# Kernel tuning notes

Measured on AMD Instinct MI355X. Metric: run time of the kernel, lower is better.

## Reference

```python
import jax, jax.numpy as jnp
import numpy as np

D_MODEL = 1024


def setup_inputs() -> dict:
    key = jax.random.key(0)
    kx, kq, kk, kv = jax.random.split(key, 4)
    x = jax.random.normal(kx, (4, 2048, D_MODEL), dtype=jnp.float32)
    s = 1.0 / np.sqrt(D_MODEL)
    # torch nn.Linear weight is [out, in]; y = x @ W.T
    Wq = jax.random.normal(kq, (D_MODEL, D_MODEL), dtype=jnp.float32) * s
    Wk = jax.random.normal(kk, (D_MODEL, D_MODEL), dtype=jnp.float32) * s
    Wv = jax.random.normal(kv, (D_MODEL, D_MODEL), dtype=jnp.float32) * s
    return {"x": x, "Wq": Wq, "Wk": Wk, "Wv": Wv}


def reference(x, Wq, Wk, Wv):
    # Linear projections (no bias): [b, s, d]
    Q = jnp.einsum("bsd,ed->bse", x, Wq)
    K = jnp.einsum("bsd,ed->bse", x, Wk)
    V = jnp.einsum("bsd,ed->bse", x, Wv)
    d_k = Q.shape[-1]
    scores = jnp.einsum("bqd,bkd->bqk", Q, K) / jnp.sqrt(jnp.asarray(d_k, Q.dtype))
    weights = jax.nn.softmax(scores, axis=-1)
    return jnp.einsum("bqk,bkd->bqd", weights, V)
```

## Files before the change

kernel.cpp:

```cpp
#include <hip/hip_runtime.h>
#include <hip/hip_bf16.h>

using bf16 = __hip_bfloat16;
typedef __attribute__((ext_vector_type(8))) short short8;
typedef __attribute__((ext_vector_type(16))) float f32x16;

__global__ __launch_bounds__(256) void cast_all(const float* __restrict__ x,
                                                const float* __restrict__ Wq,
                                                const float* __restrict__ Wk,
                                                const float* __restrict__ Wv,
                                                bf16* __restrict__ xb, bf16* __restrict__ Wb) {
  const int b = blockIdx.x;
  const float* src;
  bf16* dst;
  if (b < 8192) {
    src = x + (size_t)b * 1024;
    dst = xb + (size_t)b * 1024;
  } else if (b < 9216) {
    src = Wq + (size_t)(b - 8192) * 1024;
    dst = Wb + (size_t)(b - 8192) * 1024;
  } else if (b < 10240) {
    src = Wk + (size_t)(b - 9216) * 1024;
    dst = Wb + (size_t)(b - 8192) * 1024;
  } else {
    src = Wv + (size_t)(b - 10240) * 1024;
    dst = Wb + (size_t)(b - 8192) * 1024;
  }
  const int i = threadIdx.x * 4;
  const float4 f = *(const float4*)(src + i);
  bf16 h[4];
  h[0] = __float2bfloat16(f.x);
  h[1] = __float2bfloat16(f.y);
  h[2] = __float2bfloat16(f.z);
  h[3] = __float2bfloat16(f.w);
  *(uint2*)(dst + i) = *(const uint2*)h;
}

#define GPHASE(AS, BS, Q, S0, S1, VM)                                          \
  do {                                                                         \
    short8 af[4], bv[2];                                                       \
    _Pragma("unroll") for (int mt = 0; mt < 4; ++mt) {                         \
      const int row = wr * 128 + mt * 32 + rl;                                 \
      const int fz = (row + (row >> 2)) & 3;                                   \
      af[mt] = *(const short8*)((AS) + row * 32 + ((((Q)*2 + grp) ^ fz) << 3));\
    }                                                                          \
    _Pragma("unroll") for (int nt = 0; nt < 2; ++nt) {                         \
      const int row = wc * 64 + nt * 32 + rl;                                  \
      const int fz = (row + (row >> 2)) & 3;                                   \
      bv[nt] = *(const short8*)((BS) + row * 32 + ((((Q)*2 + grp) ^ fz) << 3));\
    }                                                                          \
    S0;                                                                        \
    S1;                                                                        \
    VM;                                                                        \
    __builtin_amdgcn_s_barrier();                                              \
    asm volatile("s_waitcnt lgkmcnt(0)" ::: "memory");                         \
    __builtin_amdgcn_sched_barrier(0);                                         \
    __builtin_amdgcn_s_setprio(1);                                             \
    _Pragma("unroll") for (int mt = 0; mt < 4; ++mt)                           \
      _Pragma("unroll") for (int nt = 0; nt < 2; ++nt)                         \
        acc[mt][nt] = __builtin_amdgcn_mfma_f32_32x32x16_bf16(af[mt], bv[nt],  \
                                                              acc[mt][nt], 0, 0, 0); \
    __builtin_amdgcn_s_setprio(0);                                             \
    __builtin_amdgcn_s_barrier();                                              \
  } while (0)

template <class Epi>
__device__ __forceinline__ void gemm256(const bf16* __restrict__ A, const bf16* __restrict__ B,
                                        int lda, int ldb, int K, int m0, int n0, Epi epi) {
  __shared__ char smem[131072];
  const int t = threadIdx.x;
  const int lane = t & 63;
  const int wave = t >> 6;
  const int wr = wave >> 2;
  const int wc = wave & 3;
  const int rl = lane & 31;
  const int grp = lane >> 5;

  f32x16 acc[4][2];
#pragma unroll
  for (int i = 0; i < 4; ++i)
#pragma unroll
    for (int j = 0; j < 2; ++j)
#pragma unroll
      for (int r = 0; r < 16; ++r) acc[i][j][r] = 0.f;

  const bf16* gA[2];
  const bf16* gB[2];
#pragma unroll
  for (int h = 0; h < 2; ++h) {
    const int row = h * 128 + (t >> 2);
    const int fz = (row + (row >> 2)) & 3;
    const int c = ((t & 3) ^ fz) << 3;
    gA[h] = A + (size_t)(m0 + row) * lda + c;
    gB[h] = B + (size_t)(n0 + row) * ldb + c;
  }

  const int NT = K >> 5;

  auto stageA = [&](int kt, int h) {
    char* dst = smem + (((kt & 3) * 2048 + h * 512 + wave * 64) << 4);
    __builtin_amdgcn_global_load_lds(
        (const __attribute__((address_space(1))) unsigned int*)(gA[h] + kt * 32),
        (__attribute__((address_space(3))) unsigned int*)dst, 16, 0, 0);
  };
  auto stageB = [&](int kt, int h) {
    char* dst = smem + (((kt & 3) * 2048 + 1024 + h * 512 + wave * 64) << 4);
    __builtin_amdgcn_global_load_lds(
        (const __attribute__((address_space(1))) unsigned int*)(gB[h] + kt * 32),
        (__attribute__((address_space(3))) unsigned int*)dst, 16, 0, 0);
  };

  stageA(0, 0); stageB(0, 0); stageA(0, 1); stageB(0, 1);
  stageA(1, 0); stageB(1, 0); stageA(1, 1); stageB(1, 1);
  stageA(2, 0); stageB(2, 0); stageA(2, 1); stageB(2, 1);
  asm volatile("s_waitcnt vmcnt(8)" ::: "memory");
  __builtin_amdgcn_s_barrier();

  for (int kt = 0; kt < NT; ++kt) {
    const bf16* As = (const bf16*)(smem + (kt & 3) * 32768);
    const bf16* Bs = (const bf16*)(smem + (kt & 3) * 32768 + 16384);
    const bool pre = (kt + 3 < NT);
    GPHASE(As, Bs, 0, if (pre) stageA(kt + 3, 0), if (pre) stageB(kt + 3, 0), ((void)0));
    GPHASE(As, Bs, 1, if (pre) stageA(kt + 3, 1), if (pre) stageB(kt + 3, 1),
           asm volatile("s_waitcnt vmcnt(8)" ::: "memory"));
  }
  __syncthreads();

  epi(acc, m0, n0, wr, wc, lane, (char*)smem);
}

__device__ __forceinline__ int c_row(int reg, int lane) {
  return (reg & 3) + 8 * (reg >> 2) + 4 * (lane >> 5);
}

template <class F>
__device__ __forceinline__ void for_each_c(const f32x16 (&acc)[4][2], int wr, int wc, int lane,
                                           F f) {
  const int rl = lane & 31;
#pragma unroll
  for (int mt = 0; mt < 4; ++mt)
#pragma unroll
    for (int nt = 0; nt < 2; ++nt)
#pragma unroll
      for (int reg = 0; reg < 16; ++reg)
        f(wr * 128 + mt * 32 + c_row(reg, lane), wc * 64 + nt * 32 + rl, acc[mt][nt][reg]);
}

__global__ __launch_bounds__(512, 2) void proj_kernel(const bf16* __restrict__ xb,
                                                      const bf16* __restrict__ Wb,
                                                      bf16* __restrict__ Qb,
                                                      bf16* __restrict__ Kb,
                                                      bf16* __restrict__ Vt) {
  const int id = blockIdx.x;
  const int g = id & 7, s = id >> 3;
  const int m0 = (g * 4 + (s & 3)) * 256;
  const int n0 = (s >> 2) * 256;
  gemm256(xb, Wb, 1024, 1024, 1024, m0, n0,
          [=](const f32x16 (&acc)[4][2], int m0, int n0, int wr, int wc, int lane, char* smem) {
    if (n0 < 2048) {
      bf16* dst = (n0 < 1024) ? Qb : Kb;
      const int nb = n0 & 1023;
      for_each_c(acc, wr, wc, lane, [&](int m, int n, float v) {
        dst[(size_t)(m0 + m) * 1024 + nb + n] = __float2bfloat16(v);
      });
    } else {
      const int wave = threadIdx.x >> 6;
      bf16* T = (bf16*)smem + wave * 4352;
      const int rl = lane & 31;
      const int g4 = 4 * (lane >> 5);
      const int mbase = m0 + wr * 128;
      const int bb = mbase >> 11;
      const int sbase = mbase & 2047;
      const int nvbase = n0 - 2048 + wc * 64;
#pragma unroll
      for (int p = 0; p < 2; ++p) {
#pragma unroll
        for (int mt = 0; mt < 4; ++mt)
#pragma unroll
          for (int q = 0; q < 4; ++q) {
            bf16 h4[4];
#pragma unroll
            for (int r = 0; r < 4; ++r) h4[r] = __float2bfloat16(acc[mt][p][4 * q + r]);
            *(uint2*)(T + rl * 136 + mt * 32 + 8 * q + g4) = *(const uint2*)h4;
          }
        asm volatile("s_waitcnt lgkmcnt(0)" ::: "memory");
#pragma unroll
        for (int i = 0; i < 8; ++i) {
          const int nl = i * 4 + (lane >> 4);
          const int ml = (lane & 15) * 8;
          const short8 val = *(const short8*)(T + nl * 136 + ml);
          *(short8*)(Vt + ((size_t)bb * 1024 + nvbase + p * 32 + nl) * 2048 + sbase + ml) = val;
        }
        asm volatile("s_waitcnt lgkmcnt(0)" ::: "memory");
      }
    }
  });
}

__global__ __launch_bounds__(512, 2) void qk_exp_kernel(const bf16* __restrict__ Qb,
                                                        const bf16* __restrict__ Kb,
                                                        bf16* __restrict__ E,
                                                        float* __restrict__ Lpart) {
  const int z = blockIdx.y;
  const int id2 = blockIdx.x;
  const int g = id2 & 7, s = id2 >> 3;
  const int m0 = ((g & 3) * 2 + (s & 1)) * 256;
  const int n0 = ((g >> 2) * 4 + (s >> 1)) * 256;
  const bf16* A = Qb + (size_t)z * 2048 * 1024;
  const bf16* B = Kb + (size_t)z * 2048 * 1024;
  bf16* Ez = E + (size_t)z * 2048 * 2048;
  float* Lz = Lpart + (size_t)z * 8 * 2048;
  gemm256(A, B, 1024, 1024, 1024, m0, n0,
          [=](const f32x16 (&acc)[4][2], int m0, int n0, int wr, int wc, int lane, char* smem) {
    float* Lp = (float*)smem;
    const int rl = lane & 31;
#pragma unroll
    for (int mt = 0; mt < 4; ++mt)
#pragma unroll
      for (int reg = 0; reg < 16; ++reg) {
        const int mr = wr * 128 + mt * 32 + c_row(reg, lane);
        float s2 = 0.f;
#pragma unroll
        for (int nt = 0; nt < 2; ++nt) {
          const float e = __expf(acc[mt][nt][reg] * 0.03125f);
          Ez[(size_t)(m0 + mr) * 2048 + n0 + wc * 64 + nt * 32 + rl] = __float2bfloat16(e);
          s2 += e;
        }
        s2 += __shfl_xor(s2, 1, 64);
        s2 += __shfl_xor(s2, 2, 64);
        s2 += __shfl_xor(s2, 4, 64);
        s2 += __shfl_xor(s2, 8, 64);
        s2 += __shfl_xor(s2, 16, 64);
        if (rl == 0) Lp[mr * 4 + wc] = s2;
      }
    __syncthreads();
    const int t = threadIdx.x;
    if (t < 256)
      Lz[(n0 >> 8) * 2048 + m0 + t] = Lp[t * 4 + 0] + Lp[t * 4 + 1] + Lp[t * 4 + 2] + Lp[t * 4 + 3];
  });
}

__global__ __launch_bounds__(512, 2) void pv_kernel(const bf16* __restrict__ E,
                                                    const bf16* __restrict__ Vt,
                                                    const float* __restrict__ Lpart,
                                                    float* __restrict__ out) {
  const int z = blockIdx.y;
  const int id2 = blockIdx.x;
  const int g = id2 & 7, s = id2 >> 3;
  const int m0 = ((g & 3) * 2 + (s & 1)) * 256;
  const int n0 = ((g >> 2) * 2 + (s >> 1)) * 256;
  const bf16* A = E + (size_t)z * 2048 * 2048;
  const bf16* B = Vt + (size_t)z * 1024 * 2048;
  const float* Lz = Lpart + (size_t)z * 8 * 2048;
  float* oz = out + (size_t)z * 2048 * 1024;
  gemm256(A, B, 2048, 2048, 2048, m0, n0,
          [=](const f32x16 (&acc)[4][2], int m0, int n0, int wr, int wc, int lane, char* smem) {
    float* Lsm = (float*)smem;
    const int t = threadIdx.x;
    if (t < 256) {
      float s2 = 0.f;
#pragma unroll
      for (int i = 0; i < 8; ++i) s2 += Lz[(size_t)i * 2048 + m0 + t];
      Lsm[t] = 1.f / s2;
    }
    __syncthreads();
    const int rl = lane & 31;
#pragma unroll
    for (int mt = 0; mt < 4; ++mt)
#pragma unroll
      for (int reg = 0; reg < 16; ++reg) {
        const int ml = wr * 128 + mt * 32 + c_row(reg, lane);
        const float il = Lsm[ml];
#pragma unroll
        for (int nt = 0; nt < 2; ++nt)
          oz[(size_t)(m0 + ml) * 1024 + n0 + wc * 64 + nt * 32 + rl] = acc[mt][nt][reg] * il;
      }
  });
}

extern "C" void kernel_launch(void* const* d_in, const int* in_sizes, int n_in,
                              void* d_out, int out_size, void* d_ws, size_t ws_size,
                              hipStream_t stream) {
  const float* x = (const float*)d_in[0];
  const float* Wq = (const float*)d_in[1];
  const float* Wk = (const float*)d_in[2];
  const float* Wv = (const float*)d_in[3];
  float* out = (float*)d_out;

  char* w = (char*)d_ws;
  bf16* xb = (bf16*)w; w += (size_t)8192 * 1024 * 2;
  bf16* Wb = (bf16*)w; w += (size_t)3072 * 1024 * 2;
  bf16* Qb = (bf16*)w; w += (size_t)8192 * 1024 * 2;
  bf16* Kb = (bf16*)w; w += (size_t)8192 * 1024 * 2;
  bf16* Vt = (bf16*)w; w += (size_t)8192 * 1024 * 2;
  bf16* E  = (bf16*)w; w += (size_t)4 * 2048 * 2048 * 2;
  float* Lpart = (float*)w; w += (size_t)4 * 8 * 2048 * 4;

  cast_all<<<11264, 256, 0, stream>>>(x, Wq, Wk, Wv, xb, Wb);

  proj_kernel<<<384, 512, 0, stream>>>(xb, Wb, Qb, Kb, Vt);

  qk_exp_kernel<<<dim3(64, 4), 512, 0, stream>>>(Qb, Kb, E, Lpart);

  pv_kernel<<<dim3(32, 4), 512, 0, stream>>>(E, Vt, Lpart, out);
}
```

Before: 261.6 us.

## Restructure GEMM mainloop into 64-wide K tiles with 4-phase double-buffered schedule

Replaces the 4-stage, 32-wide-K pipeline with a double-buffered 64-wide-K scheme. Each K tile is split into four MFMA quadrants, and the A/B half-tile loads for the next tiles are interleaved between them. Each wave's rows are remapped to two 64-row halves, so the epilogues and the V-transpose staging buffer change to match. The aim is fewer barriers and better overlap of LDS reads, global-to-LDS loads and MFMA work, at the cost of more register pressure and more complex wait-count bookkeeping.

After: 255.4 us. 2.4% less time.

```diff
diff --git a/kernel.cpp b/kernel.cpp
--- a/kernel.cpp
+++ b/kernel.cpp
@@ -36,33 +36,11 @@
   *(uint2*)(dst + i) = *(const uint2*)h;
 }
 
-#define GPHASE(AS, BS, Q, S0, S1, VM)                                          \
-  do {                                                                         \
-    short8 af[4], bv[2];                                                       \
-    _Pragma("unroll") for (int mt = 0; mt < 4; ++mt) {                         \
-      const int row = wr * 128 + mt * 32 + rl;                                 \
-      const int fz = (row + (row >> 2)) & 3;                                   \
-      af[mt] = *(const short8*)((AS) + row * 32 + ((((Q)*2 + grp) ^ fz) << 3));\
-    }                                                                          \
-    _Pragma("unroll") for (int nt = 0; nt < 2; ++nt) {                         \
-      const int row = wc * 64 + nt * 32 + rl;                                  \
-      const int fz = (row + (row >> 2)) & 3;                                   \
-      bv[nt] = *(const short8*)((BS) + row * 32 + ((((Q)*2 + grp) ^ fz) << 3));\
-    }                                                                          \
-    S0;                                                                        \
-    S1;                                                                        \
-    VM;                                                                        \
-    __builtin_amdgcn_s_barrier();                                              \
-    asm volatile("s_waitcnt lgkmcnt(0)" ::: "memory");                         \
-    __builtin_amdgcn_sched_barrier(0);                                         \
-    __builtin_amdgcn_s_setprio(1);                                             \
-    _Pragma("unroll") for (int mt = 0; mt < 4; ++mt)                           \
-      _Pragma("unroll") for (int nt = 0; nt < 2; ++nt)                         \
-        acc[mt][nt] = __builtin_amdgcn_mfma_f32_32x32x16_bf16(af[mt], bv[nt],  \
-                                                              acc[mt][nt], 0, 0, 0); \
-    __builtin_amdgcn_s_setprio(0);                                             \
-    __builtin_amdgcn_s_barrier();                                              \
-  } while (0)
+#define MM_PHASE(H, NTQ)                                                        \
+  _Pragma("unroll") for (int ks = 0; ks < 4; ++ks)                              \
+    _Pragma("unroll") for (int mtq = 0; mtq < 2; ++mtq)                         \
+      acc[(H)*2 + mtq][(NTQ)] = __builtin_amdgcn_mfma_f32_32x32x16_bf16(        \
+          af[ks][mtq], bv[ks][(NTQ)], acc[(H)*2 + mtq][(NTQ)], 0, 0, 0);
 
 template <class Epi>
 __device__ __forceinline__ void gemm256(const bf16* __restrict__ A, const bf16* __restrict__ B,
@@ -84,49 +62,100 @@
 #pragma unroll
       for (int r = 0; r < 16; ++r) acc[i][j][r] = 0.f;
 
-  const bf16* gA[2];
-  const bf16* gB[2];
-#pragma unroll
-  for (int h = 0; h < 2; ++h) {
-    const int row = h * 128 + (t >> 2);
-    const int fz = (row + (row >> 2)) & 3;
-    const int c = ((t & 3) ^ fz) << 3;
-    gA[h] = A + (size_t)(m0 + row) * lda + c;
-    gB[h] = B + (size_t)(n0 + row) * ldb + c;
-  }
-
-  const int NT = K >> 5;
-
-  auto stageA = [&](int kt, int h) {
-    char* dst = smem + (((kt & 3) * 2048 + h * 512 + wave * 64) << 4);
-    __builtin_amdgcn_global_load_lds(
-        (const __attribute__((address_space(1))) unsigned int*)(gA[h] + kt * 32),
-        (__attribute__((address_space(3))) unsigned int*)dst, 16, 0, 0);
+  const int srow = t >> 2;
+  const int sf = (srow + (srow >> 2)) & 3;
+  const int sc = ((t & 3) ^ sf) << 3;
+  const bf16* baseA = A + (size_t)(m0 + srow) * lda + sc;
+  const bf16* baseB = B + (size_t)(n0 + srow) * ldb + sc;
+
+  auto stage = [&](int mat, int h, int kt) {
+    const bf16* src = (mat ? baseB : baseA) + (size_t)h * 128 * (mat ? ldb : lda) + kt * 64;
+    char* dst = smem + (kt & 1) * 65536 + mat * 32768 + h * 8192 + wave * 1024;
+#pragma unroll
+    for (int j = 0; j < 2; ++j)
+      __builtin_amdgcn_global_load_lds(
+          (const __attribute__((address_space(1))) unsigned int*)(src + j * 32),
+          (__attribute__((address_space(3))) unsigned int*)(dst + j * 16384), 16, 0, 0);
   };
-  auto stageB = [&](int kt, int h) {
-    char* dst = smem + (((kt & 3) * 2048 + 1024 + h * 512 + wave * 64) << 4);
-    __builtin_amdgcn_global_load_lds(
-        (const __attribute__((address_space(1))) unsigned int*)(gB[h] + kt * 32),
-        (__attribute__((address_space(3))) unsigned int*)dst, 16, 0, 0);
+
+  short8 af[4][2], bv[4][2];
+
+  auto readA = [&](const char* bufA, int h) {
+#pragma unroll
+    for (int ks = 0; ks < 4; ++ks)
+#pragma unroll
+      for (int mtq = 0; mtq < 2; ++mtq) {
+        const int row = h * 128 + wr * 64 + mtq * 32 + rl;
+        const int fz = (row + (row >> 2)) & 3;
+        const int kb = (ks & 1) * 2 + grp;
+        af[ks][mtq] =
+            *(const short8*)(bufA + (ks >> 1) * 16384 + row * 64 + ((kb ^ fz) << 4));
+      }
   };
-
-  stageA(0, 0); stageB(0, 0); stageA(0, 1); stageB(0, 1);
-  stageA(1, 0); stageB(1, 0); stageA(1, 1); stageB(1, 1);
-  stageA(2, 0); stageB(2, 0); stageA(2, 1); stageB(2, 1);
-  asm volatile("s_waitcnt vmcnt(8)" ::: "memory");
+  auto readB = [&](const char* bufB) {
+#pragma unroll
+    for (int ks = 0; ks < 4; ++ks)
+#pragma unroll
+      for (int nt = 0; nt < 2; ++nt) {
+        const int row = wc * 64 + nt * 32 + rl;
+        const int fz = (row + (row >> 2)) & 3;
+        const int kb = (ks & 1) * 2 + grp;
+        bv[ks][nt] =
+            *(const short8*)(bufB + (ks >> 1) * 16384 + row * 64 + ((kb ^ fz) << 4));
+      }
+  };
+
+  const int NT = K >> 6;
+
+  stage(0, 0, 0); stage(0, 1, 0); stage(1, 0, 0); stage(1, 1, 0);
+  stage(1, 0, 1); stage(1, 1, 1); stage(0, 1, 1);
+  asm volatile("s_waitcnt vmcnt(6)" ::: "memory");
   __builtin_amdgcn_s_barrier();
+  __builtin_amdgcn_sched_barrier(0);
 
   for (int kt = 0; kt < NT; ++kt) {
-    const bf16* As = (const bf16*)(smem + (kt & 3) * 32768);
-    const bf16* Bs = (const bf16*)(smem + (kt & 3) * 32768 + 16384);
-    const bool pre = (kt + 3 < NT);
-    GPHASE(As, Bs, 0, if (pre) stageA(kt + 3, 0), if (pre) stageB(kt + 3, 0), ((void)0));
-    GPHASE(As, Bs, 1, if (pre) stageA(kt + 3, 1), if (pre) stageB(kt + 3, 1),
-           asm volatile("s_waitcnt vmcnt(8)" ::: "memory"));
+    const char* bufA = smem + (kt & 1) * 65536;
+    const char* bufB = bufA + 32768;
+    readA(bufA, 0);
+    readB(bufB);
+    if (kt + 1 < NT) stage(0, 0, kt + 1);
+    __builtin_amdgcn_s_barrier();
+    asm volatile("s_waitcnt lgkmcnt(0)" ::: "memory");
+    __builtin_amdgcn_sched_barrier(0);
+    __builtin_amdgcn_s_setprio(1);
+    MM_PHASE(0, 0)
+    __builtin_amdgcn_s_setprio(0);
+    __builtin_amdgcn_s_barrier();
+    if (kt + 2 < NT) stage(1, 0, kt + 2);
+    __builtin_amdgcn_s_barrier();
+    __builtin_amdgcn_s_setprio(1);
+    MM_PHASE(0, 1)
+    __builtin_amdgcn_s_setprio(0);
+    __builtin_amdgcn_s_barrier();
+    readA(bufA, 1);
+    if (kt + 2 < NT) stage(1, 1, kt + 2);
+    __builtin_amdgcn_s_barrier();
+    asm volatile("s_waitcnt lgkmcnt(0)" ::: "memory");
+    __builtin_amdgcn_sched_barrier(0);
+    __builtin_amdgcn_s_setprio(1);
+    MM_PHASE(1, 0)
+    __builtin_amdgcn_s_setprio(0);
+    __builtin_amdgcn_s_barrier();
+    if (kt + 2 < NT) {
+      stage(0, 1, kt + 2);
+      asm volatile("s_waitcnt vmcnt(6)" ::: "memory");
+    } else if (kt + 1 < NT) {
+      asm volatile("s_waitcnt vmcnt(0)" ::: "memory");
+    }
+    __builtin_amdgcn_s_barrier();
+    __builtin_amdgcn_s_setprio(1);
+    MM_PHASE(1, 1)
+    __builtin_amdgcn_s_setprio(0);
+    __builtin_amdgcn_s_barrier();
   }
   __syncthreads();
 
-  epi(acc, m0, n0, wr, wc, lane, (char*)smem);
+  epi(acc, m0, n0, wr, wc, lane, wave, (char*)smem);
 }
 
 __device__ __forceinline__ int c_row(int reg, int lane) {
@@ -138,12 +167,15 @@
                                            F f) {
   const int rl = lane & 31;
 #pragma unroll
-  for (int mt = 0; mt < 4; ++mt)
-#pragma unroll
-    for (int nt = 0; nt < 2; ++nt)
-#pragma unroll
-      for (int reg = 0; reg < 16; ++reg)
-        f(wr * 128 + mt * 32 + c_row(reg, lane), wc * 64 + nt * 32 + rl, acc[mt][nt][reg]);
+  for (int h = 0; h < 2; ++h)
+#pragma unroll
+    for (int mtq = 0; mtq < 2; ++mtq)
+#pragma unroll
+      for (int nt = 0; nt < 2; ++nt)
+#pragma unroll
+        for (int reg = 0; reg < 16; ++reg)
+          f(h * 128 + wr * 64 + mtq * 32 + c_row(reg, lane), wc * 64 + nt * 32 + rl,
+            acc[h * 2 + mtq][nt][reg]);
 }
 
 __global__ __launch_bounds__(512, 2) void proj_kernel(const bf16* __restrict__ xb,
@@ -156,7 +188,8 @@
   const int m0 = (g * 4 + (s & 3)) * 256;
   const int n0 = (s >> 2) * 256;
   gemm256(xb, Wb, 1024, 1024, 1024, m0, n0,
-          [=](const f32x16 (&acc)[4][2], int m0, int n0, int wr, int wc, int lane, char* smem) {
+          [=](const f32x16 (&acc)[4][2], int m0, int n0, int wr, int wc, int lane, int wave,
+              char* smem) {
     if (n0 < 2048) {
       bf16* dst = (n0 < 1024) ? Qb : Kb;
       const int nb = n0 & 1023;
@@ -164,34 +197,37 @@
         dst[(size_t)(m0 + m) * 1024 + nb + n] = __float2bfloat16(v);
       });
     } else {
-      const int wave = threadIdx.x >> 6;
-      bf16* T = (bf16*)smem + wave * 4352;
+      bf16* T = (bf16*)smem + wave * 2304;
       const int rl = lane & 31;
       const int g4 = 4 * (lane >> 5);
-      const int mbase = m0 + wr * 128;
-      const int bb = mbase >> 11;
-      const int sbase = mbase & 2047;
-      const int nvbase = n0 - 2048 + wc * 64;
-#pragma unroll
-      for (int p = 0; p < 2; ++p) {
-#pragma unroll
-        for (int mt = 0; mt < 4; ++mt)
-#pragma unroll
-          for (int q = 0; q < 4; ++q) {
-            bf16 h4[4];
-#pragma unroll
-            for (int r = 0; r < 4; ++r) h4[r] = __float2bfloat16(acc[mt][p][4 * q + r]);
-            *(uint2*)(T + rl * 136 + mt * 32 + 8 * q + g4) = *(const uint2*)h4;
+      const int nvb = n0 - 2048 + wc * 64;
+#pragma unroll
+      for (int h = 0; h < 2; ++h) {
+        const int mbase = m0 + h * 128 + wr * 64;
+        const int bb = mbase >> 11;
+        const int sbase = mbase & 2047;
+#pragma unroll
+        for (int p = 0; p < 2; ++p) {
+#pragma unroll
+          for (int mtq = 0; mtq < 2; ++mtq)
+#pragma unroll
+            for (int q = 0; q < 4; ++q) {
+              bf16 h4[4];
+#pragma unroll
+              for (int r = 0; r < 4; ++r)
+                h4[r] = __float2bfloat16(acc[h * 2 + mtq][p][4 * q + r]);
+              *(uint2*)(T + rl * 72 + mtq * 32 + 8 * q + g4) = *(const uint2*)h4;
+            }
+          asm volatile("s_waitcnt lgkmcnt(0)" ::: "memory");
+#pragma unroll
+          for (int i = 0; i < 4; ++i) {
+            const int nl = i * 8 + (lane >> 3);
+            const int ml = (lane & 7) * 8;
+            const short8 val = *(const short8*)(T + nl * 72 + ml);
+            *(short8*)(Vt + ((size_t)bb * 1024 + nvb + p * 32 + nl) * 2048 + sbase + ml) = val;
           }
-        asm volatile("s_waitcnt lgkmcnt(0)" ::: "memory");
-#pragma unroll
-        for (int i = 0; i < 8; ++i) {
-          const int nl = i * 4 + (lane >> 4);
-          const int ml = (lane & 15) * 8;
-          const short8 val = *(const short8*)(T + nl * 136 + ml);
-          *(short8*)(Vt + ((size_t)bb * 1024 + nvbase + p * 32 + nl) * 2048 + sbase + ml) = val;
+          asm volatile("s_waitcnt lgkmcnt(0)" ::: "memory");
         }
-        asm volatile("s_waitcnt lgkmcnt(0)" ::: "memory");
       }
     }
   });
@@ -211,32 +247,36 @@
   bf16* Ez = E + (size_t)z * 2048 * 2048;
   float* Lz = Lpart + (size_t)z * 8 * 2048;
   gemm256(A, B, 1024, 1024, 1024, m0, n0,
-          [=](const f32x16 (&acc)[4][2], int m0, int n0, int wr, int wc, int lane, char* smem) {
+          [=](const f32x16 (&acc)[4][2], int m0, int n0, int wr, int wc, int lane, int wave,
+              char* smem) {
     float* Lp = (float*)smem;
     const int rl = lane & 31;
 #pragma unroll
-    for (int mt = 0; mt < 4; ++mt)
-#pragma unroll
-      for (int reg = 0; reg < 16; ++reg) {
-        const int mr = wr * 128 + mt * 32 + c_row(reg, lane);
-        float s2 = 0.f;
-#pragma unroll
-        for (int nt = 0; nt < 2; ++nt) {
-          const float e = __expf(acc[mt][nt][reg] * 0.03125f);
-          Ez[(size_t)(m0 + mr) * 2048 + n0 + wc * 64 + nt * 32 + rl] = __float2bfloat16(e);
-          s2 += e;
+    for (int h = 0; h < 2; ++h)
+#pragma unroll
+      for (int mtq = 0; mtq < 2; ++mtq)
+#pragma unroll
+        for (int reg = 0; reg < 16; ++reg) {
+          const int mr = h * 128 + wr * 64 + mtq * 32 + c_row(reg, lane);
+          float s2 = 0.f;
+#pragma unroll
+          for (int nt = 0; nt < 2; ++nt) {
+            const float e = __expf(acc[h * 2 + mtq][nt][reg] * 0.03125f);
+            Ez[(size_t)(m0 + mr) * 2048 + n0 + wc * 64 + nt * 32 + rl] = __float2bfloat16(e);
+            s2 += e;
+          }
+          s2 += __shfl_xor(s2, 1, 64);
+          s2 += __shfl_xor(s2, 2, 64);
+          s2 += __shfl_xor(s2, 4, 64);
+          s2 += __shfl_xor(s2, 8, 64);
+          s2 += __shfl_xor(s2, 16, 64);
+          if (rl == 0) Lp[mr * 4 + wc] = s2;
         }
-        s2 += __shfl_xor(s2, 1, 64);
-        s2 += __shfl_xor(s2, 2, 64);
-        s2 += __shfl_xor(s2, 4, 64);
-        s2 += __shfl_xor(s2, 8, 64);
-        s2 += __shfl_xor(s2, 16, 64);
-        if (rl == 0) Lp[mr * 4 + wc] = s2;
-      }
     __syncthreads();
     const int t = threadIdx.x;
     if (t < 256)
-      Lz[(n0 >> 8) * 2048 + m0 + t] = Lp[t * 4 + 0] + Lp[t * 4 + 1] + Lp[t * 4 + 2] + Lp[t * 4 + 3];
+      Lz[(n0 >> 8) * 2048 + m0 + t] =
+          Lp[t * 4 + 0] + Lp[t * 4 + 1] + Lp[t * 4 + 2] + Lp[t * 4 + 3];
   });
 }
 
@@ -254,7 +294,8 @@
   const float* Lz = Lpart + (size_t)z * 8 * 2048;
   float* oz = out + (size_t)z * 2048 * 1024;
   gemm256(A, B, 2048, 2048, 2048, m0, n0,
-          [=](const f32x16 (&acc)[4][2], int m0, int n0, int wr, int wc, int lane, char* smem) {
+          [=](const f32x16 (&acc)[4][2], int m0, int n0, int wr, int wc, int lane, int wave,
+              char* smem) {
     float* Lsm = (float*)smem;
     const int t = threadIdx.x;
     if (t < 256) {
@@ -266,15 +307,18 @@
     __syncthreads();
     const int rl = lane & 31;
 #pragma unroll
-    for (int mt = 0; mt < 4; ++mt)
-#pragma unroll
-      for (int reg = 0; reg < 16; ++reg) {
-        const int ml = wr * 128 + mt * 32 + c_row(reg, lane);
-        const float il = Lsm[ml];
-#pragma unroll
-        for (int nt = 0; nt < 2; ++nt)
-          oz[(size_t)(m0 + ml) * 1024 + n0 + wc * 64 + nt * 32 + rl] = acc[mt][nt][reg] * il;
-      }
+    for (int h = 0; h < 2; ++h)
+#pragma unroll
+      for (int mtq = 0; mtq < 2; ++mtq)
+#pragma unroll
+        for (int reg = 0; reg < 16; ++reg) {
+          const int ml = h * 128 + wr * 64 + mtq * 32 + c_row(reg, lane);
+          const float il = Lsm[ml];
+#pragma unroll
+          for (int nt = 0; nt < 2; ++nt)
+            oz[(size_t)(m0 + ml) * 1024 + n0 + wc * 64 + nt * 32 + rl] =
+                acc[h * 2 + mtq][nt][reg] * il;
+        }
   });
 }
 
```
